# Kernel optimization log

Hardware: AMD Instinct MI355X
Metric: run time of the kernel (lower is better)

The kernel has to match this reference:

```python
import jax, jax.numpy as jnp
import numpy as np
from jax import lax

D_STATE = 16
D_CONV = 4
EPS = 1e-6


def setup_inputs() -> dict:
    key = jax.random.key(0)
    ks = jax.random.split(key, 8)
    B, L, H = 2, 2048, 1024
    d_inner = 2 * H
    s = lambda n: 1.0 / np.sqrt(n)
    x = jax.random.normal(ks[0], (B, L, H), jnp.float32)
    norm_w = jnp.ones((H,), jnp.float32)
    w_in = jax.random.normal(ks[1], (H, 2 * d_inner), jnp.float32) * s(H)
    conv_w = jax.random.normal(ks[2], (d_inner, 1, D_CONV), jnp.float32) * s(D_CONV)
    conv_b = jnp.zeros((d_inner,), jnp.float32)
    w_xproj = jax.random.normal(ks[3], (d_inner, 2 * D_STATE + d_inner), jnp.float32) * s(d_inner)
    # A_log as in torch init: log(arange(1..d_state)) broadcast over d_inner
    A_log = jnp.broadcast_to(jnp.log(jnp.arange(1, D_STATE + 1, dtype=jnp.float32)), (d_inner, D_STATE))
    D_param = jnp.ones((d_inner,), jnp.float32)
    w_out = jax.random.normal(ks[4], (d_inner, H), jnp.float32) * s(d_inner)
    return {"x": x, "norm_w": norm_w, "w_in": w_in, "conv_w": conv_w,
            "conv_b": conv_b, "w_xproj": w_xproj, "A_log": A_log,
            "D_param": D_param, "w_out": w_out}


def _rmsnorm(x, w):
    var = jnp.mean(x * x, axis=-1, keepdims=True)
    return x * lax.rsqrt(var + EPS) * w


def _silu(x):
    return x * jax.nn.sigmoid(x)


def _mamba_forward(x, norm_w, w_in, conv_w, conv_b, w_xproj, A_log, D_param, w_out):
    B, L, H = x.shape
    d_inner = w_in.shape[1] // 2
    residual = x
    h = _rmsnorm(x, norm_w)
    xz = h @ w_in                               # [B, L, 2*d_inner]
    x_ssm, z = jnp.split(xz, 2, axis=-1)
    # causal depthwise conv1d (torch pads both sides then slices -> causal left pad)
    xc = jnp.swapaxes(x_ssm, 1, 2)              # [B, d_inner, L]
    xc = jnp.pad(xc, ((0, 0), (0, 0), (D_CONV - 1, 0)))
    xc = lax.conv_general_dilated(xc, conv_w, (1,), 'VALID',
                                  feature_group_count=d_inner)
    xc = xc + conv_b[None, :, None]
    x_ssm = _silu(jnp.swapaxes(xc, 1, 2))       # [B, L, d_inner]
    proj = x_ssm @ w_xproj
    B_in = proj[..., :D_STATE]                  # [B, L, n]
    C_in = proj[..., D_STATE:2 * D_STATE]
    delta = jax.nn.softplus(proj[..., 2 * D_STATE:])  # [B, L, d_inner]
    A = -jnp.exp(A_log)                         # [d_inner, n]

    def step(hst, inp):
        xs, dt, Bt, Ct = inp                    # [B,d], [B,d], [B,n], [B,n]
        dA = jnp.exp(dt[..., None] * A)         # [B, d, n]
        hst = dA * hst + (dt * xs)[..., None] * Bt[:, None, :]
        y = jnp.einsum('bdn,bn->bd', hst, Ct)
        return hst, y

    h0 = jnp.zeros((B, d_inner, D_STATE), x_ssm.dtype)
    xs_t = jnp.swapaxes(x_ssm, 0, 1)            # [L, B, d]
    dt_t = jnp.swapaxes(delta, 0, 1)
    Bt_t = jnp.swapaxes(B_in, 0, 1)
    Ct_t = jnp.swapaxes(C_in, 0, 1)
    _, ys = lax.scan(step, h0, (xs_t, dt_t, Bt_t, Ct_t))
    y = jnp.swapaxes(ys, 0, 1)                  # [B, L, d]
    y = (y + D_param * x_ssm) * _silu(z)
    return residual + y @ w_out


def reference(x, norm_w, w_in, conv_w, conv_b, w_xproj, A_log, D_param, w_out):
    return _mamba_forward(x, norm_w, w_in, conv_w, conv_b, w_xproj, A_log, D_param, w_out)
```

## Files before the change

kernel.cpp:

```cpp
#include <hip/hip_runtime.h>
#include <math.h>

#define BATCH 2
#define LSEQ  2048
#define HDIM  1024
#define DI    2048
#define DS    16
#define NPROJ 2080
#define TOK   4096
#define XZW   4096
#define NCH   64
#define CLEN  32

typedef _Float16 f16;
typedef _Float16 f16x8 __attribute__((ext_vector_type(8)));
typedef _Float16 f16x4 __attribute__((ext_vector_type(4)));
typedef float    f32x4 __attribute__((ext_vector_type(4)));

__device__ __forceinline__ float siluf(float v) { return v / (1.f + __expf(-v)); }
__device__ __forceinline__ float softplusf(float v) {
  return v > 20.f ? v : log1pf(__expf(v));
}

__device__ __forceinline__ void gload16(const void* g, void* l) {
  __builtin_amdgcn_global_load_lds(
      (const __attribute__((address_space(1))) void*)g,
      (__attribute__((address_space(3))) void*)l, 16, 0, 0);
}

__global__ __launch_bounds__(256) void k_transpose(
    const float* __restrict__ W, f16* __restrict__ Wt, int R, int C) {
  __shared__ float t[32][33];
  int c0 = blockIdx.x * 32, r0 = blockIdx.y * 32;
  int tx = threadIdx.x & 31, ty = threadIdx.x >> 5;
#pragma unroll
  for (int i = 0; i < 4; ++i) {
    int r = ty + i * 8;
    t[r][tx] = W[(size_t)(r0 + r) * C + c0 + tx];
  }
  __syncthreads();
#pragma unroll
  for (int i = 0; i < 4; ++i) {
    int r = ty + i * 8;
    Wt[(size_t)(c0 + r) * R + r0 + tx] = (f16)t[tx][r];
  }
}

__global__ __launch_bounds__(256) void k_rmsnorm(
    const float* __restrict__ x, const float* __restrict__ w, f16* __restrict__ h) {
  int t = blockIdx.x;
  int tid = threadIdx.x;
  float4 v = reinterpret_cast<const float4*>(x + (size_t)t * HDIM)[tid];
  float ss = v.x * v.x + v.y * v.y + v.z * v.z + v.w * v.w;
#pragma unroll
  for (int off = 32; off; off >>= 1) ss += __shfl_down(ss, off, 64);
  __shared__ float sred[4];
  if ((tid & 63) == 0) sred[tid >> 6] = ss;
  __syncthreads();
  float tot = sred[0] + sred[1] + sred[2] + sred[3];
  float scale = rsqrtf(tot * (1.f / HDIM) + 1e-6f);
  float4 wv = reinterpret_cast<const float4*>(w)[tid];
  f16x4 o;
  o[0] = (f16)(v.x * scale * wv.x);
  o[1] = (f16)(v.y * scale * wv.y);
  o[2] = (f16)(v.z * scale * wv.z);
  o[3] = (f16)(v.w * scale * wv.w);
  *reinterpret_cast<f16x4*>(h + (size_t)t * HDIM + tid * 4) = o;
}

template <int MODE>
__global__ __launch_bounds__(256) void k_mgemm(
    const f16* __restrict__ A, const f16* __restrict__ Bt,
    float* __restrict__ C, const float* __restrict__ R,
    int M, int N, int K) {
  __shared__ __align__(16) f16 At[128 * 32];
  __shared__ __align__(16) f16 Bs[128 * 32];
  const int tid = threadIdx.x;
  const int lane = tid & 63;
  const int w = tid >> 6;
  const int wm = w >> 1, wn = w & 1;
  const int m0 = blockIdx.y * 128, n0 = blockIdx.x * 128;
  const int Nlim = N - 1;

  f32x4 acc[4][4];
#pragma unroll
  for (int i = 0; i < 4; ++i)
#pragma unroll
    for (int j = 0; j < 4; ++j) acc[i][j] = (f32x4){0.f, 0.f, 0.f, 0.f};

  const int fr = lane & 15;
  const int kg = (lane >> 4) << 3;

  for (int k0 = 0; k0 < K; k0 += 32) {
#pragma unroll
    for (int i = 0; i < 2; ++i) {
      const int c = w + i * 4;
      const int row = c * 16 + (lane >> 2);
      const int koffb = ((lane & 3) << 4) ^ ((row & 3) << 4);
      gload16(A + (size_t)(m0 + row) * K + k0 + (koffb >> 1),
              (char*)At + c * 1024 + (lane << 4));
      int rb = n0 + row;
      rb = rb > Nlim ? Nlim : rb;
      gload16(Bt + (size_t)rb * K + k0 + (koffb >> 1),
              (char*)Bs + c * 1024 + (lane << 4));
    }
    __syncthreads();
    f16x8 a[4], b[4];
#pragma unroll
    for (int mi = 0; mi < 4; ++mi) {
      int row = wm * 64 + mi * 16 + fr;
      a[mi] = *(const f16x8*)&At[(row << 5) + (kg ^ ((row & 3) << 3))];
    }
#pragma unroll
    for (int ni = 0; ni < 4; ++ni) {
      int row = wn * 64 + ni * 16 + fr;
      b[ni] = *(const f16x8*)&Bs[(row << 5) + (kg ^ ((row & 3) << 3))];
    }
#pragma unroll
    for (int mi = 0; mi < 4; ++mi)
#pragma unroll
      for (int ni = 0; ni < 4; ++ni)
        acc[mi][ni] = __builtin_amdgcn_mfma_f32_16x16x32_f16(
            a[mi], b[ni], acc[mi][ni], 0, 0, 0);
    __syncthreads();
  }

  const int r4 = (lane >> 4) << 2;
#pragma unroll
  for (int mi = 0; mi < 4; ++mi) {
#pragma unroll
    for (int ni = 0; ni < 4; ++ni) {
      int col = n0 + wn * 64 + ni * 16 + fr;
      if (col < N) {
        size_t base = (size_t)(m0 + wm * 64 + mi * 16 + r4) * N + col;
#pragma unroll
        for (int j = 0; j < 4; ++j) {
          float v = acc[mi][ni][j];
          if (MODE == 1 && col >= 2 * DS) v = softplusf(v);
          if (MODE == 2) v += R[base + (size_t)j * N];
          C[base + (size_t)j * N] = v;
        }
      }
    }
  }
}

__global__ __launch_bounds__(256) void k_conv(
    const float* __restrict__ xz, const float* __restrict__ cw,
    const float* __restrict__ cb, f16* __restrict__ xs) {
  size_t idx = (size_t)blockIdx.x * 256 + threadIdx.x;
  int d = (int)(idx & (DI - 1));
  size_t tf = idx >> 11;
  int t = (int)(tf & (LSEQ - 1));
  const float* base = xz + tf * XZW + d;
  float acc = cb[d];
  float w0 = cw[d * 4 + 0], w1 = cw[d * 4 + 1], w2 = cw[d * 4 + 2], w3 = cw[d * 4 + 3];
  acc = fmaf(w3, base[0], acc);
  if (t >= 1) acc = fmaf(w2, *(base - (ptrdiff_t)XZW), acc);
  if (t >= 2) acc = fmaf(w1, *(base - (ptrdiff_t)(2 * XZW)), acc);
  if (t >= 3) acc = fmaf(w0, *(base - (ptrdiff_t)(3 * XZW)), acc);
  xs[idx] = (f16)siluf(acc);
}


__global__ __launch_bounds__(256) void k_scanA(
    const float* __restrict__ proj, const f16* __restrict__ xs,
    const float* __restrict__ A_log,
    float* __restrict__ Atot, float* __restrict__ Hend) {
  int gid = blockIdx.x * 256 + threadIdx.x;
  int d = gid & (DI - 1);
  int b = (gid >> 11) & (BATCH - 1);
  int c = gid >> 12;
  float Ad[DS];
  {
    const float4* ap = reinterpret_cast<const float4*>(A_log + (size_t)d * DS);
#pragma unroll
    for (int i = 0; i < 4; ++i) {
      float4 v = ap[i];
      Ad[4 * i + 0] = -__expf(v.x);
      Ad[4 * i + 1] = -__expf(v.y);
      Ad[4 * i + 2] = -__expf(v.z);
      Ad[4 * i + 3] = -__expf(v.w);
    }
  }
  float h[DS], P[DS];
#pragma unroll
  for (int n = 0; n < DS; ++n) { h[n] = 0.f; P[n] = 1.f; }
  const float* prow = proj + ((size_t)b * LSEQ + (size_t)c * CLEN) * NPROJ;
  const f16* xrow = xs + ((size_t)b * LSEQ + (size_t)c * CLEN) * DI + d;
  for (int t = 0; t < CLEN; ++t) {
    const float* pr = prow + (size_t)t * NPROJ;
    float dt = pr[2 * DS + d];
    float xv = (float)xrow[(size_t)t * DI];
    float Bv[DS];
    {
      const float4* p4 = reinterpret_cast<const float4*>(pr);
#pragma unroll
      for (int i = 0; i < 4; ++i) {
        float4 v = p4[i];
        Bv[4 * i + 0] = v.x; Bv[4 * i + 1] = v.y;
        Bv[4 * i + 2] = v.z; Bv[4 * i + 3] = v.w;
      }
    }
    float dxv = dt * xv;
#pragma unroll
    for (int n = 0; n < DS; ++n) {
      float da = __expf(dt * Ad[n]);
      P[n] *= da;
      h[n] = fmaf(da, h[n], dxv * Bv[n]);
    }
  }
  float4* ao = reinterpret_cast<float4*>(Atot + (size_t)gid * DS);
  float4* ho = reinterpret_cast<float4*>(Hend + (size_t)gid * DS);
#pragma unroll
  for (int i = 0; i < 4; ++i) {
    ao[i] = make_float4(P[4 * i], P[4 * i + 1], P[4 * i + 2], P[4 * i + 3]);
    ho[i] = make_float4(h[4 * i], h[4 * i + 1], h[4 * i + 2], h[4 * i + 3]);
  }
}

__global__ __launch_bounds__(256) void k_scanB(
    float* __restrict__ Atot, const float* __restrict__ Hend) {
  int gid = blockIdx.x * 256 + threadIdx.x;
  float h = 0.f;
#pragma unroll
  for (int c = 0; c < NCH; ++c) {
    size_t idx = (size_t)c * (BATCH * DI * DS) + gid;
    float P = Atot[idx];
    Atot[idx] = h;
    h = fmaf(P, h, Hend[idx]);
  }
}

__global__ __launch_bounds__(256) void k_scanC(
    const float* __restrict__ proj, const f16* __restrict__ xs,
    const float* __restrict__ xz, const float* __restrict__ A_log,
    const float* __restrict__ Dp, const float* __restrict__ Hin,
    f16* __restrict__ yg) {
  int gid = blockIdx.x * 256 + threadIdx.x;
  int d = gid & (DI - 1);
  int b = (gid >> 11) & (BATCH - 1);
  int c = gid >> 12;
  float Ad[DS];
  {
    const float4* ap = reinterpret_cast<const float4*>(A_log + (size_t)d * DS);
#pragma unroll
    for (int i = 0; i < 4; ++i) {
      float4 v = ap[i];
      Ad[4 * i + 0] = -__expf(v.x);
      Ad[4 * i + 1] = -__expf(v.y);
      Ad[4 * i + 2] = -__expf(v.z);
      Ad[4 * i + 3] = -__expf(v.w);
    }
  }
  float h[DS];
  {
    const float4* hi = reinterpret_cast<const float4*>(Hin + (size_t)gid * DS);
#pragma unroll
    for (int i = 0; i < 4; ++i) {
      float4 v = hi[i];
      h[4 * i + 0] = v.x; h[4 * i + 1] = v.y;
      h[4 * i + 2] = v.z; h[4 * i + 3] = v.w;
    }
  }
  float Dd = Dp[d];
  const float* prow = proj + ((size_t)b * LSEQ + (size_t)c * CLEN) * NPROJ;
  const f16* xrow = xs + ((size_t)b * LSEQ + (size_t)c * CLEN) * DI + d;
  const float* zrow = xz + ((size_t)b * LSEQ + (size_t)c * CLEN) * XZW + DI + d;
  f16* yrow = yg + ((size_t)b * LSEQ + (size_t)c * CLEN) * DI + d;
  for (int t = 0; t < CLEN; ++t) {
    const float* pr = prow + (size_t)t * NPROJ;
    float dt = pr[2 * DS + d];
    float xv = (float)xrow[(size_t)t * DI];
    float Bv[DS], Cv[DS];
    {
      const float4* p4 = reinterpret_cast<const float4*>(pr);
#pragma unroll
      for (int i = 0; i < 4; ++i) {
        float4 v = p4[i];
        Bv[4 * i + 0] = v.x; Bv[4 * i + 1] = v.y;
        Bv[4 * i + 2] = v.z; Bv[4 * i + 3] = v.w;
      }
#pragma unroll
      for (int i = 0; i < 4; ++i) {
        float4 v = p4[4 + i];
        Cv[4 * i + 0] = v.x; Cv[4 * i + 1] = v.y;
        Cv[4 * i + 2] = v.z; Cv[4 * i + 3] = v.w;
      }
    }
    float dxv = dt * xv;
    float y = 0.f;
#pragma unroll
    for (int n = 0; n < DS; ++n) {
      float da = __expf(dt * Ad[n]);
      h[n] = fmaf(da, h[n], dxv * Bv[n]);
      y = fmaf(h[n], Cv[n], y);
    }
    float z = zrow[(size_t)t * XZW];
    yrow[(size_t)t * DI] = (f16)((y + Dd * xv) * siluf(z));
  }
}

extern "C" void kernel_launch(void* const* d_in, const int* in_sizes, int n_in,
                              void* d_out, int out_size, void* d_ws, size_t ws_size,
                              hipStream_t stream) {
  const float* x       = (const float*)d_in[0];
  const float* norm_w  = (const float*)d_in[1];
  const float* w_in    = (const float*)d_in[2];
  const float* conv_w  = (const float*)d_in[3];
  const float* conv_b  = (const float*)d_in[4];
  const float* w_xproj = (const float*)d_in[5];
  const float* A_log   = (const float*)d_in[6];
  const float* D_param = (const float*)d_in[7];
  const float* w_out   = (const float*)d_in[8];
  float* out = (float*)d_out;

  char* ws = (char*)d_ws;
  size_t off = 0;
  float* xz    = (float*)(ws + off); off += (size_t)TOK * XZW * 4;
  float* proj  = (float*)(ws + off); off += (size_t)TOK * NPROJ * 4;
  f16*   h16   = (f16*)(ws + off);   off += (size_t)TOK * HDIM * 2;
  f16*   xs16  = (f16*)(ws + off);   off += (size_t)TOK * DI * 2;
  f16*   yg16  = (f16*)(ws + off);   off += (size_t)TOK * DI * 2;
  f16*   winT  = (f16*)(ws + off);   off += (size_t)XZW * HDIM * 2;
  f16*   wxT   = (f16*)(ws + off);   off += (size_t)NPROJ * DI * 2;
  f16*   woT   = (f16*)(ws + off);   off += (size_t)HDIM * DI * 2;
  const size_t SCN = (size_t)NCH * BATCH * DI * DS;
  float* Atot  = (float*)(ws + off); off += SCN * 4;
  float* Hend  = (float*)(ws + off); off += SCN * 4;

  k_transpose<<<dim3(XZW / 32, HDIM / 32), 256, 0, stream>>>(w_in, winT, HDIM, XZW);
  k_transpose<<<dim3(NPROJ / 32, DI / 32), 256, 0, stream>>>(w_xproj, wxT, DI, NPROJ);
  k_transpose<<<dim3(HDIM / 32, DI / 32), 256, 0, stream>>>(w_out, woT, DI, HDIM);
  k_rmsnorm<<<TOK, 256, 0, stream>>>(x, norm_w, h16);
  k_mgemm<0><<<dim3(XZW / 128, TOK / 128), 256, 0, stream>>>(
      h16, winT, xz, nullptr, TOK, XZW, HDIM);
  k_conv<<<(TOK * DI) / 256, 256, 0, stream>>>(xz, conv_w, conv_b, xs16);
  k_mgemm<1><<<dim3(17, TOK / 128), 256, 0, stream>>>(
      xs16, wxT, proj, nullptr, TOK, NPROJ, DI);
  const int NTH = NCH * BATCH * DI;
  k_scanA<<<NTH / 256, 256, 0, stream>>>(proj, xs16, A_log, Atot, Hend);
  k_scanB<<<(BATCH * DI * DS) / 256, 256, 0, stream>>>(Atot, Hend);
  k_scanC<<<NTH / 256, 256, 0, stream>>>(proj, xs16, xz, A_log, D_param,
                                         Atot, yg16);
  k_mgemm<2><<<dim3(HDIM / 128, TOK / 128), 256, 0, stream>>>(
      yg16, woT, out, x, TOK, HDIM, DI);
}
```

Baseline: 461.7 us.

## Double-buffer GEMM LDS loads, swizzle blocks across XCDs, emit fp16 x/z splits

The MFMA GEMM now double-buffers its LDS tiles so the async global-to-LDS loads of the next K-slice overlap compute on the current one. Block indices are remapped so neighbouring tiles land on the same XCD for better L2 reuse. The input projection GEMM now writes x and z as separate fp16 buffers instead of one fp32 xz tensor, which halves the traffic for conv and scanC. The cost is twice the LDS per block and fp16 rounding of the z and pre-conv x values.

```diff
diff --git a/kernel.cpp b/kernel.cpp
--- a/kernel.cpp
+++ b/kernel.cpp
@@ -8,7 +8,6 @@
 #define DS    16
 #define NPROJ 2080
 #define TOK   4096
-#define XZW   4096
 #define NCH   64
 #define CLEN  32
 
@@ -72,58 +71,97 @@
 __global__ __launch_bounds__(256) void k_mgemm(
     const f16* __restrict__ A, const f16* __restrict__ Bt,
     float* __restrict__ C, const float* __restrict__ R,
+    f16* __restrict__ Ox, f16* __restrict__ Oz,
     int M, int N, int K) {
-  __shared__ __align__(16) f16 At[128 * 32];
-  __shared__ __align__(16) f16 Bs[128 * 32];
+  __shared__ __align__(16) f16 At[2 * 128 * 32];
+  __shared__ __align__(16) f16 Bs[2 * 128 * 32];
   const int tid = threadIdx.x;
   const int lane = tid & 63;
   const int w = tid >> 6;
   const int wm = w >> 1, wn = w & 1;
-  const int m0 = blockIdx.y * 128, n0 = blockIdx.x * 128;
+
+  const int gx = gridDim.x;
+  const int nwg = gx * gridDim.y;
+  const int bid = blockIdx.y * gx + blockIdx.x;
+  const int q = nwg >> 3, r = nwg & 7;
+  const int xcd = bid & 7, idx = bid >> 3;
+  const int swzb = (xcd < r ? xcd * (q + 1) : r * (q + 1) + (xcd - r) * q) + idx;
+  const int m0 = (swzb / gx) * 128, n0 = (swzb % gx) * 128;
   const int Nlim = N - 1;
 
+  const int ls = lane >> 2;
+  const int kq = lane & 3;
+  const int rowA0 = w * 16 + ls;
+  const int rowA1 = rowA0 + 64;
+  const int swz = ((kq << 4) ^ ((rowA0 & 3) << 4)) >> 1;
+  const f16* gA0 = A + (size_t)(m0 + rowA0) * K + swz;
+  const f16* gA1 = A + (size_t)(m0 + rowA1) * K + swz;
+  int rb0 = n0 + rowA0; rb0 = rb0 > Nlim ? Nlim : rb0;
+  int rb1 = n0 + rowA1; rb1 = rb1 > Nlim ? Nlim : rb1;
+  const f16* gB0 = Bt + (size_t)rb0 * K + swz;
+  const f16* gB1 = Bt + (size_t)rb1 * K + swz;
+  const int ld0 = w * 1024 + (lane << 4);
+  const int ld1 = (w + 4) * 1024 + (lane << 4);
+
+  const int fr = lane & 15;
+  const int kgb = (lane >> 4) << 4;
+  int offA[4], offB[4];
+#pragma unroll
+  for (int i = 0; i < 4; ++i) {
+    int ra = wm * 64 + i * 16 + fr;
+    offA[i] = ra * 64 + (kgb ^ ((ra & 3) << 4));
+    int rbx = wn * 64 + i * 16 + fr;
+    offB[i] = rbx * 64 + (kgb ^ ((rbx & 3) << 4));
+  }
+
   f32x4 acc[4][4];
 #pragma unroll
   for (int i = 0; i < 4; ++i)
 #pragma unroll
     for (int j = 0; j < 4; ++j) acc[i][j] = (f32x4){0.f, 0.f, 0.f, 0.f};
 
-  const int fr = lane & 15;
-  const int kg = (lane >> 4) << 3;
-
-  for (int k0 = 0; k0 < K; k0 += 32) {
-#pragma unroll
-    for (int i = 0; i < 2; ++i) {
-      const int c = w + i * 4;
-      const int row = c * 16 + (lane >> 2);
-      const int koffb = ((lane & 3) << 4) ^ ((row & 3) << 4);
-      gload16(A + (size_t)(m0 + row) * K + k0 + (koffb >> 1),
-              (char*)At + c * 1024 + (lane << 4));
-      int rb = n0 + row;
-      rb = rb > Nlim ? Nlim : rb;
-      gload16(Bt + (size_t)rb * K + k0 + (koffb >> 1),
-              (char*)Bs + c * 1024 + (lane << 4));
-    }
-    __syncthreads();
-    f16x8 a[4], b[4];
-#pragma unroll
-    for (int mi = 0; mi < 4; ++mi) {
-      int row = wm * 64 + mi * 16 + fr;
-      a[mi] = *(const f16x8*)&At[(row << 5) + (kg ^ ((row & 3) << 3))];
-    }
-#pragma unroll
-    for (int ni = 0; ni < 4; ++ni) {
-      int row = wn * 64 + ni * 16 + fr;
-      b[ni] = *(const f16x8*)&Bs[(row << 5) + (kg ^ ((row & 3) << 3))];
-    }
-#pragma unroll
-    for (int mi = 0; mi < 4; ++mi)
-#pragma unroll
-      for (int ni = 0; ni < 4; ++ni)
-        acc[mi][ni] = __builtin_amdgcn_mfma_f32_16x16x32_f16(
-            a[mi], b[ni], acc[mi][ni], 0, 0, 0);
-    __syncthreads();
-  }
+  const int nt = K >> 5;
+
+#define STAGE(buf, tt)                                                   \
+  {                                                                      \
+    const int ke = (tt) << 5;                                            \
+    gload16(gA0 + ke, (char*)At + (buf)*8192 + ld0);                     \
+    gload16(gA1 + ke, (char*)At + (buf)*8192 + ld1);                     \
+    gload16(gB0 + ke, (char*)Bs + (buf)*8192 + ld0);                     \
+    gload16(gB1 + ke, (char*)Bs + (buf)*8192 + ld1);                     \
+  }
+
+#define COMPUTE(buf)                                                     \
+  {                                                                      \
+    const char* bA = (const char*)At + (buf)*8192;                       \
+    const char* bB = (const char*)Bs + (buf)*8192;                       \
+    f16x8 a[4], b[4];                                                    \
+    _Pragma("unroll") for (int mi = 0; mi < 4; ++mi)                     \
+        a[mi] = *(const f16x8*)(bA + offA[mi]);                          \
+    _Pragma("unroll") for (int ni = 0; ni < 4; ++ni)                     \
+        b[ni] = *(const f16x8*)(bB + offB[ni]);                          \
+    _Pragma("unroll") for (int mi = 0; mi < 4; ++mi)                     \
+        _Pragma("unroll") for (int ni = 0; ni < 4; ++ni)                 \
+            acc[mi][ni] = __builtin_amdgcn_mfma_f32_16x16x32_f16(        \
+                a[mi], b[ni], acc[mi][ni], 0, 0, 0);                     \
+  }
+
+  STAGE(0, 0);
+  asm volatile("s_waitcnt vmcnt(0)" ::: "memory");
+  __builtin_amdgcn_s_barrier();
+
+  for (int t = 0; t < nt; t += 2) {
+    if (t + 1 < nt) STAGE(1, t + 1);
+    COMPUTE(0);
+    asm volatile("s_waitcnt vmcnt(0)" ::: "memory");
+    __builtin_amdgcn_s_barrier();
+    if (t + 2 < nt) STAGE(0, t + 2);
+    COMPUTE(1);
+    asm volatile("s_waitcnt vmcnt(0)" ::: "memory");
+    __builtin_amdgcn_s_barrier();
+  }
+#undef STAGE
+#undef COMPUTE
 
   const int r4 = (lane >> 4) << 2;
 #pragma unroll
@@ -132,13 +170,20 @@
     for (int ni = 0; ni < 4; ++ni) {
       int col = n0 + wn * 64 + ni * 16 + fr;
       if (col < N) {
-        size_t base = (size_t)(m0 + wm * 64 + mi * 16 + r4) * N + col;
+        int mrow = m0 + wm * 64 + mi * 16 + r4;
 #pragma unroll
         for (int j = 0; j < 4; ++j) {
           float v = acc[mi][ni][j];
-          if (MODE == 1 && col >= 2 * DS) v = softplusf(v);
-          if (MODE == 2) v += R[base + (size_t)j * N];
-          C[base + (size_t)j * N] = v;
+          if (MODE == 1) {
+            if (col >= 2 * DS) v = softplusf(v);
+            C[(size_t)(mrow + j) * N + col] = v;
+          } else if (MODE == 2) {
+            size_t o = (size_t)(mrow + j) * N + col;
+            C[o] = v + R[o];
+          } else {
+            if (col < DI) Ox[(size_t)(mrow + j) * DI + col] = (f16)v;
+            else          Oz[(size_t)(mrow + j) * DI + col - DI] = (f16)v;
+          }
         }
       }
     }
@@ -146,19 +191,19 @@
 }
 
 __global__ __launch_bounds__(256) void k_conv(
-    const float* __restrict__ xz, const float* __restrict__ cw,
+    const f16* __restrict__ xr, const float* __restrict__ cw,
     const float* __restrict__ cb, f16* __restrict__ xs) {
   size_t idx = (size_t)blockIdx.x * 256 + threadIdx.x;
   int d = (int)(idx & (DI - 1));
   size_t tf = idx >> 11;
   int t = (int)(tf & (LSEQ - 1));
-  const float* base = xz + tf * XZW + d;
+  const f16* base = xr + tf * DI + d;
   float acc = cb[d];
   float w0 = cw[d * 4 + 0], w1 = cw[d * 4 + 1], w2 = cw[d * 4 + 2], w3 = cw[d * 4 + 3];
-  acc = fmaf(w3, base[0], acc);
-  if (t >= 1) acc = fmaf(w2, *(base - (ptrdiff_t)XZW), acc);
-  if (t >= 2) acc = fmaf(w1, *(base - (ptrdiff_t)(2 * XZW)), acc);
-  if (t >= 3) acc = fmaf(w0, *(base - (ptrdiff_t)(3 * XZW)), acc);
+  acc = fmaf(w3, (float)base[0], acc);
+  if (t >= 1) acc = fmaf(w2, (float)base[-(ptrdiff_t)DI], acc);
+  if (t >= 2) acc = fmaf(w1, (float)base[-(ptrdiff_t)(2 * DI)], acc);
+  if (t >= 3) acc = fmaf(w0, (float)base[-(ptrdiff_t)(3 * DI)], acc);
   xs[idx] = (f16)siluf(acc);
 }
 
@@ -234,7 +279,7 @@
 
 __global__ __launch_bounds__(256) void k_scanC(
     const float* __restrict__ proj, const f16* __restrict__ xs,
-    const float* __restrict__ xz, const float* __restrict__ A_log,
+    const f16* __restrict__ z16, const float* __restrict__ A_log,
     const float* __restrict__ Dp, const float* __restrict__ Hin,
     f16* __restrict__ yg) {
   int gid = blockIdx.x * 256 + threadIdx.x;
@@ -266,7 +311,7 @@
   float Dd = Dp[d];
   const float* prow = proj + ((size_t)b * LSEQ + (size_t)c * CLEN) * NPROJ;
   const f16* xrow = xs + ((size_t)b * LSEQ + (size_t)c * CLEN) * DI + d;
-  const float* zrow = xz + ((size_t)b * LSEQ + (size_t)c * CLEN) * XZW + DI + d;
+  const f16* zrow = z16 + ((size_t)b * LSEQ + (size_t)c * CLEN) * DI + d;
   f16* yrow = yg + ((size_t)b * LSEQ + (size_t)c * CLEN) * DI + d;
   for (int t = 0; t < CLEN; ++t) {
     const float* pr = prow + (size_t)t * NPROJ;
@@ -296,7 +341,7 @@
       h[n] = fmaf(da, h[n], dxv * Bv[n]);
       y = fmaf(h[n], Cv[n], y);
     }
-    float z = zrow[(size_t)t * XZW];
+    float z = (float)zrow[(size_t)t * DI];
     yrow[(size_t)t * DI] = (f16)((y + Dd * xv) * siluf(z));
   }
 }
@@ -317,32 +362,33 @@
 
   char* ws = (char*)d_ws;
   size_t off = 0;
-  float* xz    = (float*)(ws + off); off += (size_t)TOK * XZW * 4;
   float* proj  = (float*)(ws + off); off += (size_t)TOK * NPROJ * 4;
+  f16*   xr16  = (f16*)(ws + off);   off += (size_t)TOK * DI * 2;
+  f16*   z16   = (f16*)(ws + off);   off += (size_t)TOK * DI * 2;
   f16*   h16   = (f16*)(ws + off);   off += (size_t)TOK * HDIM * 2;
   f16*   xs16  = (f16*)(ws + off);   off += (size_t)TOK * DI * 2;
   f16*   yg16  = (f16*)(ws + off);   off += (size_t)TOK * DI * 2;
-  f16*   winT  = (f16*)(ws + off);   off += (size_t)XZW * HDIM * 2;
+  f16*   winT  = (f16*)(ws + off);   off += (size_t)2 * DI * HDIM * 2;
   f16*   wxT   = (f16*)(ws + off);   off += (size_t)NPROJ * DI * 2;
   f16*   woT   = (f16*)(ws + off);   off += (size_t)HDIM * DI * 2;
   const size_t SCN = (size_t)NCH * BATCH * DI * DS;
   float* Atot  = (float*)(ws + off); off += SCN * 4;
   float* Hend  = (float*)(ws + off); off += SCN * 4;
 
-  k_transpose<<<dim3(XZW / 32, HDIM / 32), 256, 0, stream>>>(w_in, winT, HDIM, XZW);
+  k_transpose<<<dim3((2 * DI) / 32, HDIM / 32), 256, 0, stream>>>(w_in, winT, HDIM, 2 * DI);
   k_transpose<<<dim3(NPROJ / 32, DI / 32), 256, 0, stream>>>(w_xproj, wxT, DI, NPROJ);
   k_transpose<<<dim3(HDIM / 32, DI / 32), 256, 0, stream>>>(w_out, woT, DI, HDIM);
   k_rmsnorm<<<TOK, 256, 0, stream>>>(x, norm_w, h16);
-  k_mgemm<0><<<dim3(XZW / 128, TOK / 128), 256, 0, stream>>>(
-      h16, winT, xz, nullptr, TOK, XZW, HDIM);
-  k_conv<<<(TOK * DI) / 256, 256, 0, stream>>>(xz, conv_w, conv_b, xs16);
+  k_mgemm<3><<<dim3((2 * DI) / 128, TOK / 128), 256, 0, stream>>>(
+      h16, winT, nullptr, nullptr, xr16, z16, TOK, 2 * DI, HDIM);
+  k_conv<<<(TOK * DI) / 256, 256, 0, stream>>>(xr16, conv_w, conv_b, xs16);
   k_mgemm<1><<<dim3(17, TOK / 128), 256, 0, stream>>>(
-      xs16, wxT, proj, nullptr, TOK, NPROJ, DI);
+      xs16, wxT, proj, nullptr, nullptr, nullptr, TOK, NPROJ, DI);
   const int NTH = NCH * BATCH * DI;
   k_scanA<<<NTH / 256, 256, 0, stream>>>(proj, xs16, A_log, Atot, Hend);
   k_scanB<<<(BATCH * DI * DS) / 256, 256, 0, stream>>>(Atot, Hend);
-  k_scanC<<<NTH / 256, 256, 0, stream>>>(proj, xs16, xz, A_log, D_param,
+  k_scanC<<<NTH / 256, 256, 0, stream>>>(proj, xs16, z16, A_log, D_param,
                                          Atot, yg16);
   k_mgemm<2><<<dim3(HDIM / 128, TOK / 128), 256, 0, stream>>>(
-      yg16, woT, out, x, TOK, HDIM, DI);
-}
+      yg16, woT, out, x, nullptr, nullptr, TOK, HDIM, DI);
+}
```

Result: no change. 465.9 us (+0.9%).
